# Kernel tuning notes

Measured on AMD Instinct MI355X. Metric: run time of the kernel, lower is better.

The kernel has to match this reference:

```python
import jax, jax.numpy as jnp
import numpy as np

B = 8192
DIMS = (512, 768, 1024)
HID = 256
HEADS = 4
HD = HID // HEADS
TOPK = 8


def _layer_norm(x, g, b, eps=1e-5):
    m = x.mean(-1, keepdims=True)
    v = ((x - m) ** 2).mean(-1, keepdims=True)
    return (x - m) / jnp.sqrt(v + eps) * g + b


def setup_inputs() -> dict:
    key = jax.random.key(0)
    ks = jax.random.split(key, 16)
    inp = {}
    for i, d in enumerate(DIMS):
        inp[f"x{i}"] = jax.random.normal(ks[i], (B, d), jnp.float32)
        inp[f"Wp{i}"] = jax.random.normal(ks[3 + i], (d, HID), jnp.float32) / np.float32(np.sqrt(d))
        inp[f"bp{i}"] = jnp.zeros((HID,), jnp.float32)
        inp[f"g{i}"] = jnp.ones((HID,), jnp.float32)
        inp[f"be{i}"] = jnp.zeros((HID,), jnp.float32)
    inp["Win"] = jax.random.normal(ks[10], (HID, 3 * HID), jnp.float32) / np.float32(np.sqrt(HID))
    inp["bin_"] = jnp.zeros((3 * HID,), jnp.float32)
    inp["Wout"] = jax.random.normal(ks[11], (HID, HID), jnp.float32) / np.float32(np.sqrt(HID))
    inp["bout"] = jnp.zeros((HID,), jnp.float32)
    inp["W1"] = jax.random.normal(ks[12], (HID, HID // 2), jnp.float32) / np.float32(np.sqrt(HID))
    inp["b1"] = jnp.zeros((HID // 2,), jnp.float32)
    inp["W2"] = jax.random.normal(ks[13], (HID // 2, 1), jnp.float32) / np.float32(np.sqrt(HID // 2))
    inp["b2"] = jnp.zeros((1,), jnp.float32)
    return inp


def reference(x0, x1, x2, Wp0, bp0, g0, be0, Wp1, bp1, g1, be1, Wp2, bp2, g2, be2,
              Win, bin_, Wout, bout, W1, b1, W2, b2):
    # per-modality projection: Linear -> ReLU -> LayerNorm
    proj = [_layer_norm(jax.nn.relu(x @ Wp + bp), g, b)
            for x, Wp, bp, g, b in ((x0, Wp0, bp0, g0, be0),
                                    (x1, Wp1, bp1, g1, be1),
                                    (x2, Wp2, bp2, g2, be2))]
    seq = jnp.stack(proj, axis=1)  # [B, M=3, HID]
    # torch.nn.MultiheadAttention (batch_first, self-attention)
    qkv = seq @ Win + bin_
    q, k, v = jnp.split(qkv, 3, axis=-1)
    sh = lambda t: t.reshape(B, 3, HEADS, HD).transpose(0, 2, 1, 3)  # [B, H, M, HD]
    q, k, v = sh(q), sh(k), sh(v)
    scores = jnp.einsum('bhsd,bhtd->bhst', q, k) / np.float32(np.sqrt(HD))
    attn = jax.nn.softmax(scores, axis=-1)
    o = jnp.einsum('bhst,bhtd->bhsd', attn, v).transpose(0, 2, 1, 3).reshape(B, 3, HID)
    o = o @ Wout + bout
    fused = o.mean(axis=1)  # [B, HID]
    # row-softmaxed similarity
    sim = jax.nn.softmax(fused @ fused.T, axis=1)  # [B, B]
    vals, idx = jax.lax.top_k(sim, TOPK)  # [B, TOPK]
    # incidence matrix: diag=1 first, then H[neighbor, i] = sim[i, neighbor]
    # (scatter may overwrite the diagonal when i is in its own top-k, as in torch)
    H = jnp.eye(B, dtype=sim.dtype)
    cols = jnp.broadcast_to(jnp.arange(B)[:, None], (B, TOPK))
    H = H.at[idx, cols].set(vals)
    # fallback: empty columns get diagonal 1
    ar = jnp.arange(B)
    colsum = H.sum(axis=0)
    H = H.at[ar, ar].set(jnp.where(colsum == 0.0, 1.0, H[ar, ar]))
    # edge weight predictor: Linear -> ReLU -> Linear -> Sigmoid, clamp
    ew = jax.nn.sigmoid(jax.nn.relu(fused @ W1 + b1) @ W2 + b2)[:, 0]
    ew = jnp.clip(ew, 1e-8)
    return H, ew
```

## Files before the change

kernel.cpp:

```cpp
#include <hip/hip_runtime.h>
#include <hip/hip_bf16.h>
#include <math.h>

#define NB 8192
#define NHID 256

typedef __attribute__((ext_vector_type(8))) short short8;
typedef __attribute__((ext_vector_type(4))) float f32x4;
typedef unsigned short u16;

typedef __attribute__((address_space(3))) unsigned char* as3_u8;
typedef const __attribute__((address_space(1))) unsigned char* as1_cu8;
#define GLOAD_LDS16(g, l) \
    __builtin_amdgcn_global_load_lds((as1_cu8)(g), (as3_u8)(l), 16, 0, 0)

__global__ __launch_bounds__(256) void proj_ln_kernel(
    const float* __restrict__ x0, const float* __restrict__ Wp0, const float* __restrict__ bp0,
    const float* __restrict__ g0, const float* __restrict__ be0,
    const float* __restrict__ x1, const float* __restrict__ Wp1, const float* __restrict__ bp1,
    const float* __restrict__ g1, const float* __restrict__ be1,
    const float* __restrict__ x2, const float* __restrict__ Wp2, const float* __restrict__ bp2,
    const float* __restrict__ g2, const float* __restrict__ be2,
    float* __restrict__ seq)
{
    const int m = blockIdx.y;
    const float* x; const float* Wp; const float* bp; const float* g; const float* be; int d;
    if (m == 0)      { x = x0; Wp = Wp0; bp = bp0; g = g0; be = be0; d = 512; }
    else if (m == 1) { x = x1; Wp = Wp1; bp = bp1; g = g1; be = be1; d = 768; }
    else             { x = x2; Wp = Wp2; bp = bp2; g = g2; be = be2; d = 1024; }

    __shared__ float As[16][32];
    __shared__ float Bs[16][256];

    const int tid = threadIdx.x;
    const int tx = tid & 63;
    const int ty = tid >> 6;
    const int r0 = blockIdx.x * 32;

    float acc[8][4];
#pragma unroll
    for (int r = 0; r < 8; r++)
#pragma unroll
        for (int c = 0; c < 4; c++) acc[r][c] = 0.f;

    for (int k0 = 0; k0 < d; k0 += 16) {
        __syncthreads();
        {
            int eid = tid * 2;
            int row = eid >> 4, kk = eid & 15;
            float2 v = *(const float2*)&x[(size_t)(r0 + row) * d + k0 + kk];
            As[kk][row]     = v.x;
            As[kk + 1][row] = v.y;
        }
#pragma unroll
        for (int i = 0; i < 4; i++) {
            int f4id = i * 256 + tid;
            int kk = f4id >> 6, c4 = f4id & 63;
            *(float4*)&Bs[kk][c4 * 4] =
                *(const float4*)&Wp[(size_t)(k0 + kk) * NHID + c4 * 4];
        }
        __syncthreads();
#pragma unroll
        for (int kk = 0; kk < 16; kk++) {
            float4 a0 = *(float4*)&As[kk][ty * 8];
            float4 a1 = *(float4*)&As[kk][ty * 8 + 4];
            float4 b  = *(float4*)&Bs[kk][tx * 4];
            float ar[8] = {a0.x, a0.y, a0.z, a0.w, a1.x, a1.y, a1.z, a1.w};
            float bc[4] = {b.x, b.y, b.z, b.w};
#pragma unroll
            for (int r = 0; r < 8; r++)
#pragma unroll
                for (int c = 0; c < 4; c++)
                    acc[r][c] = fmaf(ar[r], bc[c], acc[r][c]);
        }
    }

    const int colb = tx * 4;
    float4 bpv = *(const float4*)&bp[colb];
    float4 gv  = *(const float4*)&g[colb];
    float4 bev = *(const float4*)&be[colb];
    float bpc[4] = {bpv.x, bpv.y, bpv.z, bpv.w};
    float gc[4]  = {gv.x, gv.y, gv.z, gv.w};
    float bec[4] = {bev.x, bev.y, bev.z, bev.w};

#pragma unroll
    for (int r = 0; r < 8; r++) {
        float y[4];
#pragma unroll
        for (int c = 0; c < 4; c++) y[c] = fmaxf(acc[r][c] + bpc[c], 0.f);
        float s  = y[0] + y[1] + y[2] + y[3];
        float s2 = y[0]*y[0] + y[1]*y[1] + y[2]*y[2] + y[3]*y[3];
#pragma unroll
        for (int off = 1; off < 64; off <<= 1) {
            s  += __shfl_xor(s, off);
            s2 += __shfl_xor(s2, off);
        }
        float meanv = s * (1.f / 256.f);
        float varv  = s2 * (1.f / 256.f) - meanv * meanv;
        float inv   = 1.f / sqrtf(varv + 1e-5f);
        float4 o;
        o.x = (y[0] - meanv) * inv * gc[0] + bec[0];
        o.y = (y[1] - meanv) * inv * gc[1] + bec[1];
        o.z = (y[2] - meanv) * inv * gc[2] + bec[2];
        o.w = (y[3] - meanv) * inv * gc[3] + bec[3];
        *(float4*)&seq[((size_t)(r0 + ty * 8 + r) * 3 + m) * NHID + colb] = o;
    }
}

__global__ __launch_bounds__(256) void qkv_kernel(
    const float* __restrict__ seq, const float* __restrict__ Win,
    const float* __restrict__ bin, float* __restrict__ qkv)
{
    __shared__ float As[16][128];
    __shared__ float Bs[16][128];
    const int tid = threadIdx.x;
    const int tx = tid & 15, ty = tid >> 4;
    const int c0 = blockIdx.x * 128;
    const int r0 = blockIdx.y * 128;

    float acc[8][8];
#pragma unroll
    for (int r = 0; r < 8; r++)
#pragma unroll
        for (int c = 0; c < 8; c++) acc[r][c] = 0.f;

    for (int k0 = 0; k0 < 256; k0 += 16) {
        __syncthreads();
#pragma unroll
        for (int i = 0; i < 2; i++) {
            int f4id = i * 256 + tid;
            int row = f4id >> 2, kq = (f4id & 3) << 2;
            float4 v = *(const float4*)&seq[(size_t)(r0 + row) * 256 + k0 + kq];
            As[kq + 0][row] = v.x; As[kq + 1][row] = v.y;
            As[kq + 2][row] = v.z; As[kq + 3][row] = v.w;
        }
#pragma unroll
        for (int i = 0; i < 2; i++) {
            int f4id = i * 256 + tid;
            int kk = f4id >> 5, c4 = f4id & 31;
            *(float4*)&Bs[kk][c4 * 4] =
                *(const float4*)&Win[(size_t)(k0 + kk) * 768 + c0 + c4 * 4];
        }
        __syncthreads();
#pragma unroll
        for (int kk = 0; kk < 16; kk++) {
            float4 a0 = *(float4*)&As[kk][ty * 8];
            float4 a1 = *(float4*)&As[kk][ty * 8 + 4];
            float4 b0 = *(float4*)&Bs[kk][tx * 4];
            float4 b1 = *(float4*)&Bs[kk][64 + tx * 4];
            float a[8]  = {a0.x, a0.y, a0.z, a0.w, a1.x, a1.y, a1.z, a1.w};
            float bb[8] = {b0.x, b0.y, b0.z, b0.w, b1.x, b1.y, b1.z, b1.w};
#pragma unroll
            for (int r = 0; r < 8; r++)
#pragma unroll
                for (int c = 0; c < 8; c++)
                    acc[r][c] = fmaf(a[r], bb[c], acc[r][c]);
        }
    }

    const int ca = c0 + tx * 4, cb = ca + 64;
    float4 ba  = *(const float4*)&bin[ca];
    float4 bb4 = *(const float4*)&bin[cb];
#pragma unroll
    for (int r = 0; r < 8; r++) {
        int row = r0 + ty * 8 + r;
        float4 oa = make_float4(acc[r][0] + ba.x,  acc[r][1] + ba.y,
                                acc[r][2] + ba.z,  acc[r][3] + ba.w);
        float4 ob = make_float4(acc[r][4] + bb4.x, acc[r][5] + bb4.y,
                                acc[r][6] + bb4.z, acc[r][7] + bb4.w);
        *(float4*)&qkv[(size_t)row * 768 + ca] = oa;
        *(float4*)&qkv[(size_t)row * 768 + cb] = ob;
    }
}

__global__ __launch_bounds__(256) void attn_kernel(
    const float* __restrict__ qkv, const float* __restrict__ Wout,
    const float* __restrict__ bout, const float* __restrict__ W1,
    const float* __restrict__ b1, const float* __restrict__ W2,
    const float* __restrict__ b2, u16* __restrict__ Fh, u16* __restrict__ Fl,
    float* __restrict__ ew)
{
    __shared__ float qk[4][2304];
    __shared__ float at[4][4][3][3];
    __shared__ float ol[12][256];
    __shared__ float fl[4][256];
    __shared__ float h1[4][128];

    const int tid = threadIdx.x;
    const int b0 = blockIdx.x * 4;

#pragma unroll
    for (int i = 0; i < 9; i++) {
        int f4 = i * 256 + tid;
        int lb = f4 / 576, rem = f4 - lb * 576;
        *(float4*)&qk[lb][rem * 4] =
            *(const float4*)&qkv[(size_t)(b0 + lb) * 2304 + rem * 4];
    }
    __syncthreads();

    if (tid < 144) {
        int lb = tid / 36, r = tid % 36;
        int h = r / 9, s = (r / 3) % 3, t = r % 3;
        const float* qp = &qk[lb][s * 768 + h * 64];
        const float* kp = &qk[lb][t * 768 + 256 + h * 64];
        float sum = 0.f;
#pragma unroll
        for (int dd = 0; dd < 64; dd++) sum = fmaf(qp[dd], kp[dd], sum);
        at[lb][h][s][t] = sum * 0.125f;
    }
    __syncthreads();

    if (tid < 48) {
        int lb = tid / 12, h = (tid / 3) % 4, s = tid % 3;
        float v0 = at[lb][h][s][0], v1 = at[lb][h][s][1], v2 = at[lb][h][s][2];
        float mx = fmaxf(v0, fmaxf(v1, v2));
        float e0 = expf(v0 - mx), e1 = expf(v1 - mx), e2 = expf(v2 - mx);
        float inv = 1.f / (e0 + e1 + e2);
        at[lb][h][s][0] = e0 * inv; at[lb][h][s][1] = e1 * inv; at[lb][h][s][2] = e2 * inv;
    }
    __syncthreads();

    {
        int j = tid, h = j >> 6;
#pragma unroll
        for (int lb = 0; lb < 4; lb++)
#pragma unroll
            for (int s = 0; s < 3; s++) {
                float o = at[lb][h][s][0] * qk[lb][0 * 768 + 512 + j]
                        + at[lb][h][s][1] * qk[lb][1 * 768 + 512 + j]
                        + at[lb][h][s][2] * qk[lb][2 * 768 + 512 + j];
                ol[lb * 3 + s][j] = o;
            }
    }
    __syncthreads();

    {
        const int txx = tid & 63, lbb = tid >> 6;
        float a0[4] = {0, 0, 0, 0}, a1[4] = {0, 0, 0, 0}, a2[4] = {0, 0, 0, 0};
        for (int k = 0; k < 256; k++) {
            float4 w = *(const float4*)&Wout[(size_t)k * 256 + txx * 4];
            float wv[4] = {w.x, w.y, w.z, w.w};
            float o0 = ol[lbb * 3 + 0][k], o1 = ol[lbb * 3 + 1][k], o2 = ol[lbb * 3 + 2][k];
#pragma unroll
            for (int c = 0; c < 4; c++) {
                a0[c] = fmaf(o0, wv[c], a0[c]);
                a1[c] = fmaf(o1, wv[c], a1[c]);
                a2[c] = fmaf(o2, wv[c], a2[c]);
            }
        }
        float4 bo = *(const float4*)&bout[txx * 4];
        float bc[4] = {bo.x, bo.y, bo.z, bo.w};
        float f[4];
        u16 hq[4], lq[4];
#pragma unroll
        for (int c = 0; c < 4; c++) {
            f[c] = ((a0[c] + bc[c]) + (a1[c] + bc[c]) + (a2[c] + bc[c])) * (1.f / 3.f);
            __hip_bfloat16 hb = __float2bfloat16(f[c]);
            float fh = __bfloat162float(hb);
            __hip_bfloat16 lb2 = __float2bfloat16(f[c] - fh);
            hq[c] = *(u16*)&hb;
            lq[c] = *(u16*)&lb2;
        }
        *(float4*)&fl[lbb][txx * 4] = make_float4(f[0], f[1], f[2], f[3]);
        uint2 hp, lp;
        hp.x = (unsigned)hq[0] | ((unsigned)hq[1] << 16);
        hp.y = (unsigned)hq[2] | ((unsigned)hq[3] << 16);
        lp.x = (unsigned)lq[0] | ((unsigned)lq[1] << 16);
        lp.y = (unsigned)lq[2] | ((unsigned)lq[3] << 16);
        *(uint2*)&Fh[(size_t)(b0 + lbb) * NHID + txx * 4] = hp;
        *(uint2*)&Fl[(size_t)(b0 + lbb) * NHID + txx * 4] = lp;
    }
    __syncthreads();

    {
        int lb = tid >> 6, j = tid & 63;
        float s0 = 0.f, s1 = 0.f;
        for (int k = 0; k < 256; k++) {
            float fv = fl[lb][k];
            s0 = fmaf(fv, W1[(size_t)k * 128 + j], s0);
            s1 = fmaf(fv, W1[(size_t)k * 128 + j + 64], s1);
        }
        h1[lb][j]      = fmaxf(s0 + b1[j], 0.f);
        h1[lb][j + 64] = fmaxf(s1 + b1[j + 64], 0.f);
    }
    __syncthreads();
    if (tid < 4) {
        float s = 0.f;
        for (int j = 0; j < 128; j++) s = fmaf(h1[tid][j], W2[j], s);
        s += b2[0];
        float e = 1.f / (1.f + expf(-s));
        ew[b0 + tid] = fmaxf(e, 1e-8f);
    }
}

__global__ __launch_bounds__(256) void sim_mfma_kernel(
    const u16* __restrict__ Fh, const u16* __restrict__ Fl, float* __restrict__ C)
{
    __shared__ __align__(16) unsigned char smem[32768];

    const int tid  = threadIdx.x;
    const int lane = tid & 63;
    const int w    = tid >> 6;
    const int wr   = w >> 1;
    const int wc   = w & 1;
    const int lr   = lane & 15;
    const int lg   = lane >> 4;

    const int orig = blockIdx.x;
    const int wg   = ((orig & 7) << 9) | (orig >> 3);
    const int i0   = (wg >> 6) << 7;
    const int j0   = (wg & 63) << 7;

    const int srow  = lane >> 3;
    const int sslot = (lane & 7) ^ srow;
    const int acol  = sslot * 8;

    f32x4 acc[4][4];
#pragma unroll
    for (int a = 0; a < 4; a++)
#pragma unroll
        for (int b = 0; b < 4; b++) acc[a][b] = (f32x4)0.f;

    for (int kt = 0; kt < 12; kt++) {
        const int seg  = kt >> 2;
        const int kloc = (kt & 3) << 6;
        const u16* Ag = (seg == 1) ? Fl : Fh;
        const u16* Bg = (seg == 2) ? Fl : Fh;

        __syncthreads();
#pragma unroll
        for (int i = 0; i < 4; i++) {
            const int rbase = w * 32 + i * 8;
            GLOAD_LDS16(&Ag[(size_t)(i0 + rbase + srow) * NHID + kloc + acol],
                        smem + rbase * 128);
            GLOAD_LDS16(&Bg[(size_t)(j0 + rbase + srow) * NHID + kloc + acol],
                        smem + 16384 + rbase * 128);
        }
        __syncthreads();

#pragma unroll
        for (int ks = 0; ks < 2; ks++) {
            short8 av[4], bv[4];
            const int slotx = ((ks * 4 + lg) ^ (lr & 7)) * 16;
#pragma unroll
            for (int f = 0; f < 4; f++) {
                av[f] = *(const short8*)(smem + (wr * 64 + f * 16 + lr) * 128 + slotx);
                bv[f] = *(const short8*)(smem + 16384 + (wc * 64 + f * 16 + lr) * 128 + slotx);
            }
#pragma unroll
            for (int fj = 0; fj < 4; fj++)
#pragma unroll
                for (int fi = 0; fi < 4; fi++)
                    acc[fj][fi] = __builtin_amdgcn_mfma_f32_16x16x32_bf16(
                        bv[fj], av[fi], acc[fj][fi], 0, 0, 0);
        }
    }

#pragma unroll
    for (int fj = 0; fj < 4; fj++)
#pragma unroll
        for (int fi = 0; fi < 4; fi++) {
            const int r = i0 + wr * 64 + fi * 16 + lr;
            const int c = j0 + wc * 64 + fj * 16 + lg * 4;
            *(f32x4*)&C[(size_t)r * NB + c] = acc[fj][fi];
        }
}

__global__ __launch_bounds__(256) void topk_kernel(
    float* __restrict__ logits, float* __restrict__ topv, int* __restrict__ topi)
{
    __shared__ float wv[8][4];
    __shared__ int   sidx[8];
    __shared__ float red[4];
    const int row = blockIdx.x;
    const int tid = threadIdx.x;
    float* L = &logits[(size_t)row * NB];

    if (tid < 8) sidx[tid] = 0x7fffffff;

    float v[32];
#pragma unroll
    for (int q = 0; q < 8; q++) {
        float4 x4 = *(const float4*)&L[(q * 256 + tid) * 4];
        v[q * 4 + 0] = x4.x; v[q * 4 + 1] = x4.y;
        v[q * 4 + 2] = x4.z; v[q * 4 + 3] = x4.w;
    }
    float g[8];
#pragma unroll
    for (int q = 0; q < 8; q++)
        g[q] = fmaxf(fmaxf(v[q * 4], v[q * 4 + 1]), fmaxf(v[q * 4 + 2], v[q * 4 + 3]));

    __syncthreads();

    float rank_v[8]; int rank_i[8];
#pragma unroll
    for (int r = 0; r < 8; r++) {
        float t = fmaxf(fmaxf(fmaxf(g[0], g[1]), fmaxf(g[2], g[3])),
                        fmaxf(fmaxf(g[4], g[5]), fmaxf(g[6], g[7])));
        float wm = t;
#pragma unroll
        for (int off = 1; off < 64; off <<= 1)
            wm = fmaxf(wm, __shfl_xor(wm, off));
        if ((tid & 63) == 0) wv[r][tid >> 6] = wm;
        __syncthreads();
        const float m = fmaxf(fmaxf(wv[r][0], wv[r][1]), fmaxf(wv[r][2], wv[r][3]));
        if (t == m) {
            int best = 0x7fffffff;
#pragma unroll
            for (int q = 0; q < 8; q++)
#pragma unroll
                for (int c = 0; c < 4; c++)
                    if (v[q * 4 + c] == m) {
                        int gi = (q * 256 + tid) * 4 + c;
                        best = min(best, gi);
                    }
            atomicMin(&sidx[r], best);
        }
        __syncthreads();
        const int idx = sidx[r];
        rank_v[r] = m; rank_i[r] = idx;
        if (((idx >> 2) & 255) == tid) {
            const int q = idx >> 10;
#pragma unroll
            for (int qq = 0; qq < 8; qq++) if (qq == q) {
                const int c = idx & 3;
#pragma unroll
                for (int cc = 0; cc < 4; cc++) if (cc == c)
                    v[qq * 4 + cc] = -INFINITY;
                g[qq] = fmaxf(fmaxf(v[qq * 4], v[qq * 4 + 1]),
                              fmaxf(v[qq * 4 + 2], v[qq * 4 + 3]));
            }
        }
    }

    const float mx = rank_v[0];
    float ps = 0.f;
#pragma unroll
    for (int q = 0; q < 32; q++) ps += __expf(v[q] - mx);
#pragma unroll
    for (int off = 1; off < 64; off <<= 1) ps += __shfl_xor(ps, off);
    if ((tid & 63) == 0) red[tid >> 6] = ps;
    __syncthreads();
    if (tid == 0) {
        float er[8];
        float esum = 0.f;
#pragma unroll
        for (int r = 0; r < 8; r++) { er[r] = __expf(rank_v[r] - mx); esum += er[r]; }
        const float inv = 1.f / (red[0] + red[1] + red[2] + red[3] + esum);
#pragma unroll
        for (int r = 0; r < 8; r++) {
            topv[(size_t)row * 8 + r] = er[r] * inv;
            topi[(size_t)row * 8 + r] = rank_i[r];
        }
    }

    __syncthreads();
#pragma unroll
    for (int q = 0; q < 8; q++) {
        int c4 = (q * 256 + tid) * 4;
        float4 o;
        o.x = (c4 == row)     ? 1.f : 0.f;
        o.y = (c4 + 1 == row) ? 1.f : 0.f;
        o.z = (c4 + 2 == row) ? 1.f : 0.f;
        o.w = (c4 + 3 == row) ? 1.f : 0.f;
        *(float4*)&L[c4] = o;
    }
}

__global__ __launch_bounds__(256) void scatter_kernel(
    const float* __restrict__ topv, const int* __restrict__ topi, float* __restrict__ H)
{
    int t = blockIdx.x * 256 + threadIdx.x;
    int i = t >> 3;
    H[(size_t)topi[t] * NB + i] = topv[t];
}

extern "C" void kernel_launch(void* const* d_in, const int* in_sizes, int n_in,
                              void* d_out, int out_size, void* d_ws, size_t ws_size,
                              hipStream_t stream)
{
    const float* x0  = (const float*)d_in[0];
    const float* Wp0 = (const float*)d_in[1];
    const float* bp0 = (const float*)d_in[2];
    const float* g0  = (const float*)d_in[3];
    const float* be0 = (const float*)d_in[4];
    const float* x1  = (const float*)d_in[5];
    const float* Wp1 = (const float*)d_in[6];
    const float* bp1 = (const float*)d_in[7];
    const float* g1  = (const float*)d_in[8];
    const float* be1 = (const float*)d_in[9];
    const float* x2  = (const float*)d_in[10];
    const float* Wp2 = (const float*)d_in[11];
    const float* bp2 = (const float*)d_in[12];
    const float* g2  = (const float*)d_in[13];
    const float* be2 = (const float*)d_in[14];
    const float* Win = (const float*)d_in[15];
    const float* bin = (const float*)d_in[16];
    const float* Wout= (const float*)d_in[17];
    const float* bout= (const float*)d_in[18];
    const float* W1  = (const float*)d_in[19];
    const float* b1  = (const float*)d_in[20];
    const float* W2  = (const float*)d_in[21];
    const float* b2  = (const float*)d_in[22];

    float* out = (float*)d_out;

    float* qkv = out;
    float* seq = out + 18874368;
    u16*   Fh   = (u16*)d_ws;
    u16*   Fl   = (u16*)((char*)d_ws + (4u << 20));
    float* topv = (float*)((char*)d_ws + (8u << 20));
    int*   topi = (int*)((char*)d_ws + (8u << 20) + 262144);
    float* ew   = out + (size_t)NB * NB;

    proj_ln_kernel<<<dim3(256, 3), 256, 0, stream>>>(
        x0, Wp0, bp0, g0, be0, x1, Wp1, bp1, g1, be1, x2, Wp2, bp2, g2, be2, seq);
    qkv_kernel<<<dim3(6, 192), 256, 0, stream>>>(seq, Win, bin, qkv);
    attn_kernel<<<2048, 256, 0, stream>>>(qkv, Wout, bout, W1, b1, W2, b2, Fh, Fl, ew);
    sim_mfma_kernel<<<4096, 256, 0, stream>>>(Fh, Fl, out);
    topk_kernel<<<8192, 256, 0, stream>>>(out, topv, topi);
    scatter_kernel<<<256, 256, 0, stream>>>(topv, topi, out);
}
```

Before: 970.1 us.

## Move projection and QKV GEMMs to split-bf16 MFMA with pre-transposed weights

```diff
diff --git a/kernel.cpp b/kernel.cpp
--- a/kernel.cpp
+++ b/kernel.cpp
@@ -14,162 +14,212 @@
 #define GLOAD_LDS16(g, l) \
     __builtin_amdgcn_global_load_lds((as1_cu8)(g), (as3_u8)(l), 16, 0, 0)
 
-__global__ __launch_bounds__(256) void proj_ln_kernel(
-    const float* __restrict__ x0, const float* __restrict__ Wp0, const float* __restrict__ bp0,
-    const float* __restrict__ g0, const float* __restrict__ be0,
-    const float* __restrict__ x1, const float* __restrict__ Wp1, const float* __restrict__ bp1,
-    const float* __restrict__ g1, const float* __restrict__ be1,
-    const float* __restrict__ x2, const float* __restrict__ Wp2, const float* __restrict__ bp2,
-    const float* __restrict__ g2, const float* __restrict__ be2,
-    float* __restrict__ seq)
-{
+__device__ __forceinline__ void split1(float f, u16& h, u16& l) {
+    __hip_bfloat16 hb = __float2bfloat16(f);
+    float fh = __bfloat162float(hb);
+    __hip_bfloat16 lb = __float2bfloat16(f - fh);
+    h = *(u16*)&hb; l = *(u16*)&lb;
+}
+
+__global__ __launch_bounds__(256) void wconv_kernel(
+    const float* __restrict__ Wp0, const float* __restrict__ Wp1,
+    const float* __restrict__ Wp2, const float* __restrict__ Win,
+    u16* __restrict__ WTh, u16* __restrict__ WTl,
+    u16* __restrict__ WinTh, u16* __restrict__ WinTl)
+{
+    __shared__ float Ts[32][33];
+    const int b = blockIdx.x;
+    const int tid = threadIdx.x;
+    const float* src; u16 *dh, *dl; int W, outstride, outbase, k0, c0;
+    if (b < 576) {
+        int base, koff;
+        const float* wp;
+        if (b < 128)      { base = 0;   koff = 0;    wp = Wp0; }
+        else if (b < 320) { base = 128; koff = 512;  wp = Wp1; }
+        else              { base = 320; koff = 1280; wp = Wp2; }
+        int lb = b - base;
+        k0 = (lb >> 3) * 32; c0 = (lb & 7) * 32;
+        src = wp; W = 256; dh = WTh; dl = WTl; outstride = 2304; outbase = koff;
+    } else {
+        int lb = b - 576;
+        k0 = (lb & 7) * 32; c0 = (lb >> 3) * 32;
+        src = Win; W = 768; dh = WinTh; dl = WinTl; outstride = 256; outbase = 0;
+    }
+    {
+        int r = tid >> 3, cq = (tid & 7) * 4;
+        float4 v = *(const float4*)&src[(size_t)(k0 + r) * W + c0 + cq];
+        Ts[r][cq] = v.x; Ts[r][cq + 1] = v.y; Ts[r][cq + 2] = v.z; Ts[r][cq + 3] = v.w;
+    }
+    __syncthreads();
+    {
+        int c = tid >> 3, r4 = (tid & 7) * 4;
+        ushort4 h, l;
+        split1(Ts[r4 + 0][c], h.x, l.x);
+        split1(Ts[r4 + 1][c], h.y, l.y);
+        split1(Ts[r4 + 2][c], h.z, l.z);
+        split1(Ts[r4 + 3][c], h.w, l.w);
+        size_t off = (size_t)(c0 + c) * outstride + outbase + k0 + r4;
+        *(ushort4*)&dh[off] = h;
+        *(ushort4*)&dl[off] = l;
+    }
+}
+
+__global__ __launch_bounds__(256) void proj_mfma_kernel(
+    const float* __restrict__ x0, const float* __restrict__ x1, const float* __restrict__ x2,
+    const float* __restrict__ bp0, const float* __restrict__ g0, const float* __restrict__ be0,
+    const float* __restrict__ bp1, const float* __restrict__ g1, const float* __restrict__ be1,
+    const float* __restrict__ bp2, const float* __restrict__ g2, const float* __restrict__ be2,
+    const u16* __restrict__ WTh, const u16* __restrict__ WTl,
+    u16* __restrict__ seqh, u16* __restrict__ seql)
+{
+    __shared__ __align__(16) unsigned char smem[51200];
+
     const int m = blockIdx.y;
-    const float* x; const float* Wp; const float* bp; const float* g; const float* be; int d;
-    if (m == 0)      { x = x0; Wp = Wp0; bp = bp0; g = g0; be = be0; d = 512; }
-    else if (m == 1) { x = x1; Wp = Wp1; bp = bp1; g = g1; be = be1; d = 768; }
-    else             { x = x2; Wp = Wp2; bp = bp2; g = g2; be = be2; d = 1024; }
-
-    __shared__ float As[16][32];
-    __shared__ float Bs[16][256];
+    const float* x; const float* bp; const float* g; const float* be; int d, koff;
+    if (m == 0)      { x = x0; bp = bp0; g = g0; be = be0; d = 512;  koff = 0; }
+    else if (m == 1) { x = x1; bp = bp1; g = g1; be = be1; d = 768;  koff = 512; }
+    else             { x = x2; bp = bp2; g = g2; be = be2; d = 1024; koff = 1280; }
 
     const int tid = threadIdx.x;
-    const int tx = tid & 63;
-    const int ty = tid >> 6;
-    const int r0 = blockIdx.x * 32;
-
-    float acc[8][4];
-#pragma unroll
-    for (int r = 0; r < 8; r++)
-#pragma unroll
-        for (int c = 0; c < 4; c++) acc[r][c] = 0.f;
-
-    for (int k0 = 0; k0 < d; k0 += 16) {
-        __syncthreads();
+    const int lane = tid & 63;
+    const int w  = tid >> 6;
+    const int lr = lane & 15;
+    const int lg = lane >> 4;
+    const int r0 = blockIdx.x * 64;
+
+    f32x4 acc[16];
+#pragma unroll
+    for (int nf = 0; nf < 16; nf++) acc[nf] = (f32x4)0.f;
+
+    const int nkt = d >> 5;
+    for (int kt = 0; kt < nkt; kt++) {
+        const int k0 = kt << 5;
+        __syncthreads();
+#pragma unroll
+        for (int i = 0; i < 4; i++) {
+            int id = i * 256 + tid;
+            int col = id >> 2, ks = (id & 3) * 8;
+            size_t go = (size_t)col * 2304 + koff + k0 + ks;
+            *(short8*)(smem + col * 80 + ks * 2)         = *(const short8*)&WTh[go];
+            *(short8*)(smem + 20480 + col * 80 + ks * 2) = *(const short8*)&WTl[go];
+        }
+#pragma unroll
+        for (int i = 0; i < 2; i++) {
+            int id = i * 256 + tid;
+            int row = id >> 3, kq = (id & 7) * 4;
+            float4 v = *(const float4*)&x[(size_t)(r0 + row) * d + k0 + kq];
+            ushort4 h, l;
+            split1(v.x, h.x, l.x); split1(v.y, h.y, l.y);
+            split1(v.z, h.z, l.z); split1(v.w, h.w, l.w);
+            *(ushort4*)(smem + 40960 + row * 80 + kq * 2) = h;
+            *(ushort4*)(smem + 46080 + row * 80 + kq * 2) = l;
+        }
+        __syncthreads();
+
+        short8 bvh = *(const short8*)(smem + 40960 + (w * 16 + lr) * 80 + lg * 16);
+        short8 bvl = *(const short8*)(smem + 46080 + (w * 16 + lr) * 80 + lg * 16);
+#pragma unroll
+        for (int nf = 0; nf < 16; nf++) {
+            short8 avh = *(const short8*)(smem + (nf * 16 + lr) * 80 + lg * 16);
+            short8 avl = *(const short8*)(smem + 20480 + (nf * 16 + lr) * 80 + lg * 16);
+            acc[nf] = __builtin_amdgcn_mfma_f32_16x16x32_bf16(avh, bvh, acc[nf], 0, 0, 0);
+            acc[nf] = __builtin_amdgcn_mfma_f32_16x16x32_bf16(avl, bvh, acc[nf], 0, 0, 0);
+            acc[nf] = __builtin_amdgcn_mfma_f32_16x16x32_bf16(avh, bvl, acc[nf], 0, 0, 0);
+        }
+    }
+
+    float s = 0.f, s2 = 0.f;
+#pragma unroll
+    for (int nf = 0; nf < 16; nf++) {
+        float4 bpv = *(const float4*)&bp[nf * 16 + lg * 4];
+        float bb[4] = {bpv.x, bpv.y, bpv.z, bpv.w};
+#pragma unroll
+        for (int r = 0; r < 4; r++) {
+            float y = fmaxf(acc[nf][r] + bb[r], 0.f);
+            acc[nf][r] = y;
+            s += y; s2 += y * y;
+        }
+    }
+    s  += __shfl_xor(s, 16);  s  += __shfl_xor(s, 32);
+    s2 += __shfl_xor(s2, 16); s2 += __shfl_xor(s2, 32);
+    const float meanv = s * (1.f / 256.f);
+    const float inv = 1.f / sqrtf(s2 * (1.f / 256.f) - meanv * meanv + 1e-5f);
+
+    const size_t rb = ((size_t)(r0 + w * 16 + lr) * 3 + m) * 256;
+#pragma unroll
+    for (int nf = 0; nf < 16; nf++) {
+        float4 gv  = *(const float4*)&g[nf * 16 + lg * 4];
+        float4 bev = *(const float4*)&be[nf * 16 + lg * 4];
+        float gc[4] = {gv.x, gv.y, gv.z, gv.w};
+        float bc[4] = {bev.x, bev.y, bev.z, bev.w};
+        ushort4 h, l;
+        float o0 = (acc[nf][0] - meanv) * inv * gc[0] + bc[0];
+        float o1 = (acc[nf][1] - meanv) * inv * gc[1] + bc[1];
+        float o2 = (acc[nf][2] - meanv) * inv * gc[2] + bc[2];
+        float o3 = (acc[nf][3] - meanv) * inv * gc[3] + bc[3];
+        split1(o0, h.x, l.x); split1(o1, h.y, l.y);
+        split1(o2, h.z, l.z); split1(o3, h.w, l.w);
+        *(ushort4*)&seqh[rb + nf * 16 + lg * 4] = h;
+        *(ushort4*)&seql[rb + nf * 16 + lg * 4] = l;
+    }
+}
+
+__global__ __launch_bounds__(256) void qkv_mfma_kernel(
+    const u16* __restrict__ seqh, const u16* __restrict__ seql,
+    const u16* __restrict__ WinTh, const u16* __restrict__ WinTl,
+    const float* __restrict__ bin, float* __restrict__ qkv)
+{
+    __shared__ __align__(16) unsigned char smem[51200];
+    const int tid = threadIdx.x;
+    const int lane = tid & 63;
+    const int w  = tid >> 6;
+    const int lr = lane & 15;
+    const int lg = lane >> 4;
+    const int c0 = blockIdx.x << 8;
+    const int r0 = blockIdx.y << 6;
+
+    f32x4 acc[16];
+#pragma unroll
+    for (int nf = 0; nf < 16; nf++) acc[nf] = (f32x4)0.f;
+
+    for (int kt = 0; kt < 8; kt++) {
+        const int k0 = kt << 5;
+        __syncthreads();
+#pragma unroll
+        for (int i = 0; i < 4; i++) {
+            int id = i * 256 + tid;
+            int col = id >> 2, ks = (id & 3) * 8;
+            size_t go = (size_t)(c0 + col) * 256 + k0 + ks;
+            *(short8*)(smem + col * 80 + ks * 2)         = *(const short8*)&WinTh[go];
+            *(short8*)(smem + 20480 + col * 80 + ks * 2) = *(const short8*)&WinTl[go];
+        }
         {
-            int eid = tid * 2;
-            int row = eid >> 4, kk = eid & 15;
-            float2 v = *(const float2*)&x[(size_t)(r0 + row) * d + k0 + kk];
-            As[kk][row]     = v.x;
-            As[kk + 1][row] = v.y;
-        }
-#pragma unroll
-        for (int i = 0; i < 4; i++) {
-            int f4id = i * 256 + tid;
-            int kk = f4id >> 6, c4 = f4id & 63;
-            *(float4*)&Bs[kk][c4 * 4] =
-                *(const float4*)&Wp[(size_t)(k0 + kk) * NHID + c4 * 4];
-        }
-        __syncthreads();
-#pragma unroll
-        for (int kk = 0; kk < 16; kk++) {
-            float4 a0 = *(float4*)&As[kk][ty * 8];
-            float4 a1 = *(float4*)&As[kk][ty * 8 + 4];
-            float4 b  = *(float4*)&Bs[kk][tx * 4];
-            float ar[8] = {a0.x, a0.y, a0.z, a0.w, a1.x, a1.y, a1.z, a1.w};
-            float bc[4] = {b.x, b.y, b.z, b.w};
-#pragma unroll
-            for (int r = 0; r < 8; r++)
-#pragma unroll
-                for (int c = 0; c < 4; c++)
-                    acc[r][c] = fmaf(ar[r], bc[c], acc[r][c]);
-        }
-    }
-
-    const int colb = tx * 4;
-    float4 bpv = *(const float4*)&bp[colb];
-    float4 gv  = *(const float4*)&g[colb];
-    float4 bev = *(const float4*)&be[colb];
-    float bpc[4] = {bpv.x, bpv.y, bpv.z, bpv.w};
-    float gc[4]  = {gv.x, gv.y, gv.z, gv.w};
-    float bec[4] = {bev.x, bev.y, bev.z, bev.w};
-
-#pragma unroll
-    for (int r = 0; r < 8; r++) {
-        float y[4];
-#pragma unroll
-        for (int c = 0; c < 4; c++) y[c] = fmaxf(acc[r][c] + bpc[c], 0.f);
-        float s  = y[0] + y[1] + y[2] + y[3];
-        float s2 = y[0]*y[0] + y[1]*y[1] + y[2]*y[2] + y[3]*y[3];
-#pragma unroll
-        for (int off = 1; off < 64; off <<= 1) {
-            s  += __shfl_xor(s, off);
-            s2 += __shfl_xor(s2, off);
-        }
-        float meanv = s * (1.f / 256.f);
-        float varv  = s2 * (1.f / 256.f) - meanv * meanv;
-        float inv   = 1.f / sqrtf(varv + 1e-5f);
-        float4 o;
-        o.x = (y[0] - meanv) * inv * gc[0] + bec[0];
-        o.y = (y[1] - meanv) * inv * gc[1] + bec[1];
-        o.z = (y[2] - meanv) * inv * gc[2] + bec[2];
-        o.w = (y[3] - meanv) * inv * gc[3] + bec[3];
-        *(float4*)&seq[((size_t)(r0 + ty * 8 + r) * 3 + m) * NHID + colb] = o;
-    }
-}
-
-__global__ __launch_bounds__(256) void qkv_kernel(
-    const float* __restrict__ seq, const float* __restrict__ Win,
-    const float* __restrict__ bin, float* __restrict__ qkv)
-{
-    __shared__ float As[16][128];
-    __shared__ float Bs[16][128];
-    const int tid = threadIdx.x;
-    const int tx = tid & 15, ty = tid >> 4;
-    const int c0 = blockIdx.x * 128;
-    const int r0 = blockIdx.y * 128;
-
-    float acc[8][8];
-#pragma unroll
-    for (int r = 0; r < 8; r++)
-#pragma unroll
-        for (int c = 0; c < 8; c++) acc[r][c] = 0.f;
-
-    for (int k0 = 0; k0 < 256; k0 += 16) {
-        __syncthreads();
-#pragma unroll
-        for (int i = 0; i < 2; i++) {
-            int f4id = i * 256 + tid;
-            int row = f4id >> 2, kq = (f4id & 3) << 2;
-            float4 v = *(const float4*)&seq[(size_t)(r0 + row) * 256 + k0 + kq];
-            As[kq + 0][row] = v.x; As[kq + 1][row] = v.y;
-            As[kq + 2][row] = v.z; As[kq + 3][row] = v.w;
-        }
-#pragma unroll
-        for (int i = 0; i < 2; i++) {
-            int f4id = i * 256 + tid;
-            int kk = f4id >> 5, c4 = f4id & 31;
-            *(float4*)&Bs[kk][c4 * 4] =
-                *(const float4*)&Win[(size_t)(k0 + kk) * 768 + c0 + c4 * 4];
-        }
-        __syncthreads();
-#pragma unroll
-        for (int kk = 0; kk < 16; kk++) {
-            float4 a0 = *(float4*)&As[kk][ty * 8];
-            float4 a1 = *(float4*)&As[kk][ty * 8 + 4];
-            float4 b0 = *(float4*)&Bs[kk][tx * 4];
-            float4 b1 = *(float4*)&Bs[kk][64 + tx * 4];
-            float a[8]  = {a0.x, a0.y, a0.z, a0.w, a1.x, a1.y, a1.z, a1.w};
-            float bb[8] = {b0.x, b0.y, b0.z, b0.w, b1.x, b1.y, b1.z, b1.w};
-#pragma unroll
-            for (int r = 0; r < 8; r++)
-#pragma unroll
-                for (int c = 0; c < 8; c++)
-                    acc[r][c] = fmaf(a[r], bb[c], acc[r][c]);
-        }
-    }
-
-    const int ca = c0 + tx * 4, cb = ca + 64;
-    float4 ba  = *(const float4*)&bin[ca];
-    float4 bb4 = *(const float4*)&bin[cb];
-#pragma unroll
-    for (int r = 0; r < 8; r++) {
-        int row = r0 + ty * 8 + r;
-        float4 oa = make_float4(acc[r][0] + ba.x,  acc[r][1] + ba.y,
-                                acc[r][2] + ba.z,  acc[r][3] + ba.w);
-        float4 ob = make_float4(acc[r][4] + bb4.x, acc[r][5] + bb4.y,
-                                acc[r][6] + bb4.z, acc[r][7] + bb4.w);
-        *(float4*)&qkv[(size_t)row * 768 + ca] = oa;
-        *(float4*)&qkv[(size_t)row * 768 + cb] = ob;
+            int row = tid >> 2, ks = (tid & 3) * 8;
+            size_t go = (size_t)(r0 + row) * 256 + k0 + ks;
+            *(short8*)(smem + 40960 + row * 80 + ks * 2) = *(const short8*)&seqh[go];
+            *(short8*)(smem + 46080 + row * 80 + ks * 2) = *(const short8*)&seql[go];
+        }
+        __syncthreads();
+
+        short8 bvh = *(const short8*)(smem + 40960 + (w * 16 + lr) * 80 + lg * 16);
+        short8 bvl = *(const short8*)(smem + 46080 + (w * 16 + lr) * 80 + lg * 16);
+#pragma unroll
+        for (int nf = 0; nf < 16; nf++) {
+            short8 avh = *(const short8*)(smem + (nf * 16 + lr) * 80 + lg * 16);
+            short8 avl = *(const short8*)(smem + 20480 + (nf * 16 + lr) * 80 + lg * 16);
+            acc[nf] = __builtin_amdgcn_mfma_f32_16x16x32_bf16(avh, bvh, acc[nf], 0, 0, 0);
+            acc[nf] = __builtin_amdgcn_mfma_f32_16x16x32_bf16(avl, bvh, acc[nf], 0, 0, 0);
+            acc[nf] = __builtin_amdgcn_mfma_f32_16x16x32_bf16(avh, bvl, acc[nf], 0, 0, 0);
+        }
+    }
+
+    const size_t rb = (size_t)(r0 + w * 16 + lr) * 768 + c0;
+#pragma unroll
+    for (int nf = 0; nf < 16; nf++) {
+        float4 bv = *(const float4*)&bin[c0 + nf * 16 + lg * 4];
+        float4 o = make_float4(acc[nf][0] + bv.x, acc[nf][1] + bv.y,
+                               acc[nf][2] + bv.z, acc[nf][3] + bv.w);
+        *(float4*)&qkv[rb + nf * 16 + lg * 4] = o;
     }
 }
 
@@ -255,11 +305,7 @@
 #pragma unroll
         for (int c = 0; c < 4; c++) {
             f[c] = ((a0[c] + bc[c]) + (a1[c] + bc[c]) + (a2[c] + bc[c])) * (1.f / 3.f);
-            __hip_bfloat16 hb = __float2bfloat16(f[c]);
-            float fh = __bfloat162float(hb);
-            __hip_bfloat16 lb2 = __float2bfloat16(f[c] - fh);
-            hq[c] = *(u16*)&hb;
-            lq[c] = *(u16*)&lb2;
+            split1(f[c], hq[c], lq[c]);
         }
         *(float4*)&fl[lbb][txx * 4] = make_float4(f[0], f[1], f[2], f[3]);
         uint2 hp, lp;
@@ -504,18 +550,25 @@
     const float* b2  = (const float*)d_in[22];
 
     float* out = (float*)d_out;
-
-    float* qkv = out;
-    float* seq = out + 18874368;
+    char*  outc = (char*)d_out;
+
+    float* qkv   = out;
+    u16*   seqh  = (u16*)(outc + 75497472);
+    u16*   seql  = (u16*)(outc + 88080384);
+    u16*   WTh   = (u16*)(outc + 100663296);
+    u16*   WTl   = (u16*)(outc + 101842944);
+    u16*   WinTh = (u16*)(outc + 103022592);
+    u16*   WinTl = (u16*)(outc + 103415808);
     u16*   Fh   = (u16*)d_ws;
     u16*   Fl   = (u16*)((char*)d_ws + (4u << 20));
     float* topv = (float*)((char*)d_ws + (8u << 20));
     int*   topi = (int*)((char*)d_ws + (8u << 20) + 262144);
     float* ew   = out + (size_t)NB * NB;
 
-    proj_ln_kernel<<<dim3(256, 3), 256, 0, stream>>>(
-        x0, Wp0, bp0, g0, be0, x1, Wp1, bp1, g1, be1, x2, Wp2, bp2, g2, be2, seq);
-    qkv_kernel<<<dim3(6, 192), 256, 0, stream>>>(seq, Win, bin, qkv);
+    wconv_kernel<<<768, 256, 0, stream>>>(Wp0, Wp1, Wp2, Win, WTh, WTl, WinTh, WinTl);
+    proj_mfma_kernel<<<dim3(128, 3), 256, 0, stream>>>(
+        x0, x1, x2, bp0, g0, be0, bp1, g1, be1, bp2, g2, be2, WTh, WTl, seqh, seql);
+    qkv_mfma_kernel<<<dim3(3, 384), 256, 0, stream>>>(seqh, seql, WinTh, WinTl, bin, qkv);
     attn_kernel<<<2048, 256, 0, stream>>>(qkv, Wout, bout, W1, b1, W2, b2, Fh, Fl, ew);
     sim_mfma_kernel<<<4096, 256, 0, stream>>>(Fh, Fl, out);
     topk_kernel<<<8192, 256, 0, stream>>>(out, topv, topi);
```

Measured after the change: 824.9 us. 1.18x faster.
